# Kernel tuning notes

Hardware: AMD Instinct MI355X
Metric: run time of the kernel (lower is better)

The kernel has to match this reference:

```python
import jax, jax.numpy as jnp
import numpy as np

N = 50000  # nodes per ntype (must be equal across ntypes per the module's forward)
E = 400000  # edges per relation

# relation order matches __init__: (src_ntype, dst_ntype)
RELS = [("stock","financial"),("stock","macro"),("stock","news"),("stock","policy"),
        ("financial","macro"),("financial","stock"),("financial","news"),("financial","policy"),
        ("macro","stock"),("macro","financial"),("macro","news"),("macro","policy"),
        ("news","stock"),("news","financial"),("news","macro"),("news","policy"),
        ("policy","stock"),("policy","macro"),("policy","news"),("policy","financial")]
NTYPES = ["stock","financial","macro","news","policy"]


def graph_conv(x_src, src, dst, W, b):
    # DGL GraphConv, norm='both': h = D_in^{-1/2} A D_out^{-1/2} x W + b
    ones = jnp.ones((src.shape[0],), x_src.dtype)
    deg_out = jax.ops.segment_sum(ones, src, num_segments=N)
    norm_s = jax.lax.rsqrt(jnp.maximum(deg_out, 1.0))
    h = x_src * norm_s[:, None]
    if W.shape[0] > W.shape[1]:  # mult W first when in_feats > out_feats
        h = h @ W
        agg = jax.ops.segment_sum(h[src], dst, num_segments=N)
    else:
        agg = jax.ops.segment_sum(h[src], dst, num_segments=N)
        agg = agg @ W
    deg_in = jax.ops.segment_sum(ones, dst, num_segments=N)
    norm_d = jax.lax.rsqrt(jnp.maximum(deg_in, 1.0))
    return agg * norm_d[:, None] + b


def hetero_layer(feats, edges, W_per_rel, b_per_rel):
    # sum-aggregate per destination ntype (aggregate='sum')
    out = {nt: jnp.zeros((N, b_per_rel[0].shape[0]), jnp.float32) for nt in NTYPES}
    for r, (s_nt, d_nt) in enumerate(RELS):
        out[d_nt] = out[d_nt] + graph_conv(feats[s_nt], edges[r, 0], edges[r, 1], W_per_rel[r], b_per_rel[r])
    return out


def setup_inputs() -> dict:
    key = jax.random.key(0)
    ks = jax.random.split(key, 16)
    H, C = 128, 10
    d = {
        "x_stock": jax.random.normal(ks[0], (N, 5), jnp.float32),
        "x_financial": jax.random.normal(ks[1], (N, 16), jnp.float32),
        "x_macro": jax.random.normal(ks[2], (N, 21), jnp.float32),
        "x_news": jax.random.normal(ks[3], (N, 768), jnp.float32),
        "x_policy": jax.random.normal(ks[4], (N, 768), jnp.float32),
        "W1_stock": jax.random.normal(ks[5], (4, 5, H), jnp.float32) * 0.1,
        "W1_financial": jax.random.normal(ks[6], (4, 16, H), jnp.float32) * 0.1,
        "W1_macro": jax.random.normal(ks[7], (4, 21, H), jnp.float32) * 0.1,
        "W1_news": jax.random.normal(ks[8], (4, 768, H), jnp.float32) * 0.02,
        "W1_policy": jax.random.normal(ks[9], (4, 768, H), jnp.float32) * 0.02,
        "b1": jnp.zeros((20, H), jnp.float32),
        "W2": jax.random.normal(ks[10], (20, H, H), jnp.float32) * 0.05,
        "b2": jnp.zeros((20, H), jnp.float32),
        "Wfc": jax.random.normal(ks[11], (H, C), jnp.float32) * 0.05,
        "bfc": jnp.zeros((C,), jnp.float32),
        "edges": jax.random.randint(ks[12], (20, 2, E), 0, N, dtype=jnp.int32),
    }
    return d


def reference(x_stock, x_financial, x_macro, x_news, x_policy,
              W1_stock, W1_financial, W1_macro, W1_news, W1_policy, b1,
              W2, b2, Wfc, bfc, edges):
    feats = {"stock": x_stock, "financial": x_financial, "macro": x_macro,
             "news": x_news, "policy": x_policy}
    # layer-1 weights in relation order (RELS grouped by src ntype, 4 each)
    W1_by_src = {"stock": W1_stock, "financial": W1_financial, "macro": W1_macro,
                 "news": W1_news, "policy": W1_policy}
    W1_list = [W1_by_src[s][r % 4] for r, (s, _) in enumerate(RELS)]
    b1_list = [b1[r] for r in range(20)]
    h1 = hetero_layer(feats, edges, W1_list, b1_list)
    W2_list = [W2[r] for r in range(20)]
    b2_list = [b2[r] for r in range(20)]
    h2 = hetero_layer(h1, edges, W2_list, b2_list)
    # manual cross-ntype accumulation into stock buffer, then divide by #ntypes
    acc = h2["stock"]
    for nt in NTYPES:
        if nt != "stock":
            acc = acc + h2[nt]
    acc = acc / len(NTYPES)
    # dgl.mean_nodes over a single graph -> [1, H]
    m = jnp.mean(acc, axis=0, keepdims=True)
    out = m @ Wfc + bfc
    return (m, out)
```

## Files before the change

### kernel.cpp

```cpp
#include <hip/hip_runtime.h>

#define NN 50000
#define EE 400000

#define CH_H 32768
#define NCH_H 2
#define ESL_H 2
#define EPS_H (EE/ESL_H)
#define I4_H (EPS_H/4)

#define ESL_C 4
#define EPS_C (EE/ESL_C)
#define I4_C (EPS_C/4)

#define CH_D 8192
#define NCH_D 7
#define ESL_D 2
#define EPS_D (EE/ESL_D)
#define I4_D (EPS_D/4)

#define NZ 261
#define ZROWS 192

#define VCH 96

__constant__ int DSTT[20]     = {1,2,3,4, 2,0,3,4, 0,1,3,4, 0,1,2,4, 0,2,3,1};
__constant__ int KIDX[20]     = {0,0,0,0, 1,0,1,1, 1,1,2,2, 2,2,2,3, 3,3,3,3};
__constant__ int DSTREL[5][4] = {{5,8,12,16},{0,9,13,19},{1,4,14,17},{2,6,10,18},{3,7,11,15}};
__constant__ int FEATS[5]     = {5, 16, 21, 768, 768};

#define OFF_HIST 0
#define OFF_CRAW 0
#define OFF_CC4  0
#define OFF_C    4000000
#define OFF_ND   5000000
#define OFF_PART 0
#define OFF_YS   6500000
#define OFF_S    6600000
#define OFF_V    6700000
#define OFF_NS   7000000
#define OFF_DACC 8000000
#define DSLICE   4000000
#define OFF_Y    8000000
#define OFF_MP   8110000
#define TOTAL_ELEMS 16000000

static __device__ __forceinline__ void fma4(float4& a, const float4& x, float w) {
    a.x += w * x.x; a.y += w * x.y; a.z += w * x.z; a.w += w * x.w;
}

__global__ __launch_bounds__(1024) void k_hist(const int* __restrict__ edges, int* __restrict__ hist_part) {
    __shared__ int h[CH_H];
    const int slice = blockIdx.x, chunk = blockIdx.y;
    const int r = blockIdx.z % 20, arr = blockIdx.z / 20;
    for (int i = threadIdx.x; i < CH_H; i += 1024) h[i] = 0;
    __syncthreads();
    const int4* key = (const int4*)(edges + (size_t)(r*2 + arr)*EE + slice*EPS_H);
    const int base = chunk * CH_H;
    for (int i = threadIdx.x; i < I4_H; i += 1024) {
        int4 k4 = key[i];
        unsigned a = (unsigned)(k4.x - base), b = (unsigned)(k4.y - base);
        unsigned c = (unsigned)(k4.z - base), d = (unsigned)(k4.w - base);
        if (a < CH_H) atomicAdd(&h[a], 1);
        if (b < CH_H) atomicAdd(&h[b], 1);
        if (c < CH_H) atomicAdd(&h[c], 1);
        if (d < CH_H) atomicAdd(&h[d], 1);
    }
    __syncthreads();
    int* outp = hist_part + (arr*ESL_H + slice)*1000000 + r*NN;
    for (int i = threadIdx.x; i < CH_H; i += 1024) {
        int u = base + i;
        if (u < NN) outp[u] = h[i];
    }
}

__global__ __launch_bounds__(256) void k_norms(const int* __restrict__ hist_part,
                                               float* __restrict__ ns, float* __restrict__ nd) {
    int r = blockIdx.y;
    int u = blockIdx.x * 256 + threadIdx.x;
    if (u >= NN) return;
    int idx = r*NN + u;
    float dop = (float)(hist_part[idx] + hist_part[1000000 + idx]);
    float dip = (float)(hist_part[2000000 + idx] + hist_part[3000000 + idx]);
    if (dop < 1.f) dop = 1.f;
    if (dip < 1.f) dip = 1.f;
    ns[idx] = 1.0f / sqrtf(dop);
    nd[idx] = 1.0f / sqrtf(dip);
}

__global__ __launch_bounds__(1024) void k_craw(const int* __restrict__ edges,
                                               const float* __restrict__ nd, float* __restrict__ craw_part) {
    __shared__ float h[CH_H];
    const int slice = blockIdx.x, chunk = blockIdx.y, r = blockIdx.z;
    for (int i = threadIdx.x; i < CH_H; i += 1024) h[i] = 0.f;
    __syncthreads();
    const int4* s4 = (const int4*)(edges + (size_t)(r*2)*EE + slice*EPS_C);
    const int4* d4 = (const int4*)(edges + (size_t)(r*2+1)*EE + slice*EPS_C);
    const float* ndr = nd + r*NN;
    const int base = chunk * CH_H;
    for (int i = threadIdx.x; i < I4_C; i += 1024) {
        int4 s = s4[i];
        int4 d = d4[i];
        unsigned a = (unsigned)(s.x - base), b = (unsigned)(s.y - base);
        unsigned c = (unsigned)(s.z - base), e = (unsigned)(s.w - base);
        if (a < CH_H) atomicAdd(&h[a], ndr[d.x]);
        if (b < CH_H) atomicAdd(&h[b], ndr[d.y]);
        if (c < CH_H) atomicAdd(&h[c], ndr[d.z]);
        if (e < CH_H) atomicAdd(&h[e], ndr[d.w]);
    }
    __syncthreads();
    float* outp = craw_part + slice*1000000 + r*NN;
    for (int i = threadIdx.x; i < CH_H; i += 1024) {
        int u = base + i;
        if (u < NN) outp[u] = h[i];
    }
}

__global__ __launch_bounds__(256) void k_cS(const float* __restrict__ craw_part, const float* __restrict__ ns,
                                            float* __restrict__ c, float* __restrict__ S) {
    int r = blockIdx.y;
    int u = blockIdx.x * 256 + threadIdx.x;
    float val = 0.f;
    if (u < NN) {
        int idx = r*NN + u;
        val = ns[idx] * (craw_part[idx] + craw_part[1000000 + idx]
                       + craw_part[2000000 + idx] + craw_part[3000000 + idx]);
        c[idx] = val;
    }
    for (int off = 32; off > 0; off >>= 1) val += __shfl_down(val, off, 64);
    __shared__ float red[4];
    if ((threadIdx.x & 63) == 0) red[threadIdx.x >> 6] = val;
    __syncthreads();
    if (threadIdx.x == 0) atomicAdd(&S[r], red[0] + red[1] + red[2] + red[3]);
}

__global__ __launch_bounds__(256) void k_cc(const float* __restrict__ c, const float* __restrict__ nd,
                                            float* __restrict__ cc4) {
    int r1 = blockIdx.y;
    int u = blockIdx.x * 256 + threadIdx.x;
    if (u >= NN) return;
    float ndv = nd[r1*NN + u];
    int d1 = DSTT[r1];
    float4 w;
    w.x = c[(4*d1+0)*NN + u] * ndv;
    w.y = c[(4*d1+1)*NN + u] * ndv;
    w.z = c[(4*d1+2)*NN + u] * ndv;
    w.w = c[(4*d1+3)*NN + u] * ndv;
    *(float4*)(cc4 + (size_t)(r1*NN + u) * 4) = w;
}

__global__ __launch_bounds__(1024) void k_dacc(const int* __restrict__ edges,
                                               const float* __restrict__ cc4, float* __restrict__ dacc_part) {
    __shared__ float h4[CH_D * 4];
    const int slice = blockIdx.x, chunk = blockIdx.y, r = blockIdx.z;
    for (int i = threadIdx.x; i < CH_D * 4; i += 1024) h4[i] = 0.f;
    __syncthreads();
    const int4* s4 = (const int4*)(edges + (size_t)(r*2)*EE + slice*EPS_D);
    const int4* d4 = (const int4*)(edges + (size_t)(r*2+1)*EE + slice*EPS_D);
    const float* ccr = cc4 + (size_t)r*NN*4;
    const int base = chunk * CH_D;
    for (int i = threadIdx.x; i < I4_D; i += 1024) {
        int4 s = s4[i];
        int4 d = d4[i];
        unsigned a = (unsigned)(s.x - base), b = (unsigned)(s.y - base);
        unsigned c = (unsigned)(s.z - base), e = (unsigned)(s.w - base);
        if (a < CH_D) {
            const float4 w = *(const float4*)(ccr + (size_t)d.x * 4);
            atomicAdd(&h4[a*4+0], w.x); atomicAdd(&h4[a*4+1], w.y);
            atomicAdd(&h4[a*4+2], w.z); atomicAdd(&h4[a*4+3], w.w);
        }
        if (b < CH_D) {
            const float4 w = *(const float4*)(ccr + (size_t)d.y * 4);
            atomicAdd(&h4[b*4+0], w.x); atomicAdd(&h4[b*4+1], w.y);
            atomicAdd(&h4[b*4+2], w.z); atomicAdd(&h4[b*4+3], w.w);
        }
        if (c < CH_D) {
            const float4 w = *(const float4*)(ccr + (size_t)d.z * 4);
            atomicAdd(&h4[c*4+0], w.x); atomicAdd(&h4[c*4+1], w.y);
            atomicAdd(&h4[c*4+2], w.z); atomicAdd(&h4[c*4+3], w.w);
        }
        if (e < CH_D) {
            const float4 w = *(const float4*)(ccr + (size_t)d.w * 4);
            atomicAdd(&h4[e*4+0], w.x); atomicAdd(&h4[e*4+1], w.y);
            atomicAdd(&h4[e*4+2], w.z); atomicAdd(&h4[e*4+3], w.w);
        }
    }
    __syncthreads();
    const int d1 = DSTT[r], kk = KIDX[r];
    float* op = dacc_part + slice * DSLICE;
#pragma unroll
    for (int j = 0; j < 4; ++j) {
        int p = 4*(4*d1 + j) + kk;
        float* pj = op + (size_t)p*NN;
        for (int i = threadIdx.x; i < CH_D; i += 1024) {
            int u = base + i;
            if (u < NN) pj[u] = h4[i*4 + j];
        }
    }
}

__global__ __launch_bounds__(192) void k_y_big(const float* __restrict__ xn, const float* __restrict__ xp,
        const float* __restrict__ ns, const float* __restrict__ dacc, float* __restrict__ partial) {
    __shared__ float wlds[64 * 8];
    const int tid = threadIdx.x;
    const int z = blockIdx.x, half = blockIdx.y, group = blockIdx.z;
    const int s1 = 3 + group;
    const float* x = (group == 0) ? xn : xp;
    const int c0 = tid * 4;
    float4 acc[8];
#pragma unroll
    for (int q = 0; q < 8; ++q) acc[q] = make_float4(0.f, 0.f, 0.f, 0.f);

    for (int t = 0; t < 3; ++t) {
        const int u0 = z * ZROWS + t * 64;
        __syncthreads();
        for (int tt = tid; tt < 512; tt += 192) {
            int ql = tt >> 6, ri = tt & 63;
            int i = half*2 + (ql >> 2), j = ql & 3;
            int r1 = 4*s1 + i;
            int p = 4*(4*DSTT[r1] + j) + KIDX[r1];
            int u = u0 + ri;
            float w = 0.f;
            if (u < NN) {
                int idx = p*NN + u;
                w = ns[r1*NN + u] * (dacc[idx] + dacc[DSLICE + idx]);
            }
            wlds[ri*8 + ql] = w;
        }
        __syncthreads();
        const int rmax = (NN - u0 < 64) ? (NN - u0) : 64;
#pragma unroll 4
        for (int ri = 0; ri < rmax; ++ri) {
            const float4 xv = *(const float4*)(x + (size_t)(u0 + ri) * 768 + c0);
            const float4 wa = *(const float4*)(wlds + ri * 8);
            const float4 wb = *(const float4*)(wlds + ri * 8 + 4);
            fma4(acc[0], xv, wa.x); fma4(acc[1], xv, wa.y);
            fma4(acc[2], xv, wa.z); fma4(acc[3], xv, wa.w);
            fma4(acc[4], xv, wb.x); fma4(acc[5], xv, wb.y);
            fma4(acc[6], xv, wb.z); fma4(acc[7], xv, wb.w);
        }
    }
    float* pslot = partial + (size_t)(z*4 + group*2 + half) * 6144;
#pragma unroll
    for (int ql = 0; ql < 8; ++ql)
        *(float4*)(pslot + ql * 768 + c0) = acc[ql];
}

template<int F>
__global__ __launch_bounds__(256) void k_y_small(const float* __restrict__ x,
        const float* __restrict__ ns, const float* __restrict__ dacc,
        float* __restrict__ ys, int s1) {
    const int q = blockIdx.x;
    const int i = q >> 2, j = q & 3;
    const int r1 = 4*s1 + i;
    const int p = 4*(4*DSTT[r1] + j) + KIDX[r1];
    const float* nsp = ns + r1*NN;
    const float* d0 = dacc + (size_t)p*NN;
    const float* d1 = d0 + DSLICE;
    float acc[F];
#pragma unroll
    for (int f = 0; f < F; ++f) acc[f] = 0.f;
    const int u0 = blockIdx.y * 6250;
    for (int u = u0 + threadIdx.x; u < u0 + 6250; u += 256) {
        float w = nsp[u] * (d0[u] + d1[u]);
        const float* xr = x + (size_t)u * F;
#pragma unroll
        for (int f = 0; f < F; ++f) acc[f] += w * xr[f];
    }
#pragma unroll
    for (int f = 0; f < F; ++f)
        for (int off = 32; off > 0; off >>= 1) acc[f] += __shfl_down(acc[f], off, 64);
    __shared__ float red[F];
    if (threadIdx.x < F) red[threadIdx.x] = 0.f;
    __syncthreads();
    if ((threadIdx.x & 63) == 0) {
#pragma unroll
        for (int f = 0; f < F; ++f) atomicAdd(&red[f], acc[f]);
    }
    __syncthreads();
    if (threadIdx.x < F) atomicAdd(&ys[p*768 + threadIdx.x], red[threadIdx.x]);
}

__global__ __launch_bounds__(768) void k_red_y(const float* __restrict__ partial,
                                               const float* __restrict__ ys, float* __restrict__ y) {
    const int p = blockIdx.x;
    const int f = threadIdx.x;
    const int r2 = p >> 2, k = p & 3;
    const int r1 = DSTREL[r2 >> 2][k];
    const int s1 = r1 >> 2;
    float s = ys[p*768 + f];
    if (s1 >= 3) {
        const int group = s1 - 3;
        const int i = r1 & 3;
        const int half = i >> 1;
        const int ql = (i & 1) * 4 + (r2 & 3);
        const float* base = partial + (size_t)(group*2 + half) * 6144 + ql * 768 + f;
        for (int z = 0; z < NZ; ++z) s += base[(size_t)z * 4 * 6144];
    }
    y[p*768 + f] = s;
}

__global__ __launch_bounds__(128) void k_v(const float* __restrict__ y,
        const float* __restrict__ W1s, const float* __restrict__ W1f, const float* __restrict__ W1m,
        const float* __restrict__ W1n, const float* __restrict__ W1p, float* __restrict__ v) {
    const int r2 = blockIdx.x;
    const int k  = blockIdx.y;
    const int fc = blockIdx.z;
    const int c  = threadIdx.x;
    const int r1 = DSTREL[r2 >> 2][k];
    const int s1 = r1 >> 2;
    const int F  = FEATS[s1];
    const int f0 = fc * VCH;
    if (f0 >= F) return;
    const int f1 = (f0 + VCH < F) ? (f0 + VCH) : F;
    const float* W1 = (s1 == 0 ? W1s : s1 == 1 ? W1f : s1 == 2 ? W1m : s1 == 3 ? W1n : W1p)
                      + (size_t)(r1 & 3) * F * 128;
    const float* yp = y + (r2*4 + k) * 768;
    float sum = 0.f;
#pragma unroll 4
    for (int f = f0; f < f1; ++f) sum += yp[f] * W1[(size_t)f * 128 + c];
    atomicAdd(&v[r2 * 128 + c], sum);
}

__global__ __launch_bounds__(128) void k_m(const float* __restrict__ v, const float* __restrict__ S,
        const float* __restrict__ b1, const float* __restrict__ W2, float* __restrict__ mpart) {
    int r2 = blockIdx.x;
    int c = threadIdx.x;
    __shared__ float vp[128];
    int s2 = r2 >> 2;
    float b = b1[DSTREL[s2][0]*128 + c] + b1[DSTREL[s2][1]*128 + c]
            + b1[DSTREL[s2][2]*128 + c] + b1[DSTREL[s2][3]*128 + c];
    vp[c] = v[r2*128 + c] + S[r2] * b;
    __syncthreads();
    const float* W2r = W2 + r2 * 16384;
    float sum = 0.f;
    for (int k = 0; k < 128; ++k) sum += vp[k] * W2r[k * 128 + c];
    mpart[r2 * 128 + c] = sum;
}

__global__ __launch_bounds__(128) void k_out(const float* __restrict__ mpart, const float* __restrict__ b2,
        const float* __restrict__ Wfc, const float* __restrict__ bfc, float* __restrict__ out) {
    int c = threadIdx.x;
    __shared__ float ml[128];
    float bs = 0.f, ms = 0.f;
    for (int r2 = 0; r2 < 20; ++r2) { bs += b2[r2 * 128 + c]; ms += mpart[r2 * 128 + c]; }
    float m = (ms + (float)NN * bs) * (1.0f / (5.0f * (float)NN));
    out[c] = m;
    ml[c] = m;
    __syncthreads();
    if (c < 10) {
        float o = bfc[c];
        for (int k = 0; k < 128; ++k) o += ml[k] * Wfc[k * 10 + c];
        out[128 + c] = o;
    }
}

extern "C" void kernel_launch(void* const* d_in, const int* in_sizes, int n_in,
                              void* d_out, int out_size, void* d_ws, size_t ws_size,
                              hipStream_t stream) {
    (void)in_sizes; (void)n_in; (void)out_size;
    const float* xs  = (const float*)d_in[0];
    const float* xf  = (const float*)d_in[1];
    const float* xm  = (const float*)d_in[2];
    const float* xn  = (const float*)d_in[3];
    const float* xp  = (const float*)d_in[4];
    const float* W1s = (const float*)d_in[5];
    const float* W1f = (const float*)d_in[6];
    const float* W1m = (const float*)d_in[7];
    const float* W1n = (const float*)d_in[8];
    const float* W1p = (const float*)d_in[9];
    const float* b1  = (const float*)d_in[10];
    const float* W2  = (const float*)d_in[11];
    const float* b2  = (const float*)d_in[12];
    const float* Wfc = (const float*)d_in[13];
    const float* bfc = (const float*)d_in[14];
    const int* edges = (const int*)d_in[15];
    float* ws = (float*)d_ws;
    int* wsi = (int*)d_ws;
    float* out = (float*)d_out;
    if (ws_size < (size_t)TOTAL_ELEMS * 4) return;

    dim3 t256(256), nb(196, 20);

    hipMemsetAsync(ws + OFF_YS, 0, (size_t)(OFF_S + 64 - OFF_YS) * 4, stream);
    hipMemsetAsync(ws + OFF_V, 0, 2560 * 4, stream);

    k_hist<<<dim3(ESL_H, NCH_H, 40), dim3(1024), 0, stream>>>(edges, wsi + OFF_HIST);
    k_norms<<<nb, t256, 0, stream>>>(wsi + OFF_HIST, ws + OFF_NS, ws + OFF_ND);
    k_craw<<<dim3(ESL_C, NCH_H, 20), dim3(1024), 0, stream>>>(edges, ws + OFF_ND, ws + OFF_CRAW);
    k_cS<<<nb, t256, 0, stream>>>(ws + OFF_CRAW, ws + OFF_NS, ws + OFF_C, ws + OFF_S);
    k_cc<<<nb, t256, 0, stream>>>(ws + OFF_C, ws + OFF_ND, ws + OFF_CC4);
    k_dacc<<<dim3(ESL_D, NCH_D, 20), dim3(1024), 0, stream>>>(edges, ws + OFF_CC4, ws + OFF_DACC);
    k_y_big<<<dim3(NZ, 2, 2), dim3(192), 0, stream>>>(xn, xp, ws + OFF_NS, ws + OFF_DACC, ws + OFF_PART);
    k_y_small<5><<<dim3(16, 8), t256, 0, stream>>>(xs, ws + OFF_NS, ws + OFF_DACC, ws + OFF_YS, 0);
    k_y_small<16><<<dim3(16, 8), t256, 0, stream>>>(xf, ws + OFF_NS, ws + OFF_DACC, ws + OFF_YS, 1);
    k_y_small<21><<<dim3(16, 8), t256, 0, stream>>>(xm, ws + OFF_NS, ws + OFF_DACC, ws + OFF_YS, 2);
    k_red_y<<<dim3(80), dim3(768), 0, stream>>>(ws + OFF_PART, ws + OFF_YS, ws + OFF_Y);
    k_v<<<dim3(20, 4, 8), dim3(128), 0, stream>>>(ws + OFF_Y, W1s, W1f, W1m, W1n, W1p, ws + OFF_V);
    k_m<<<dim3(20), dim3(128), 0, stream>>>(ws + OFF_V, ws + OFF_S, b1, W2, ws + OFF_MP);
    k_out<<<dim3(1), dim3(128), 0, stream>>>(ws + OFF_MP, b2, Wfc, bfc, out);
}
```

Measured before the change: 963.3 us.

## Use direct global atomics for dacc and fuse y_big halves into one pass

The shared-memory chunked histogram in the dacc stage, which rescanned the edge lists once per chunk and wrote two partial slices, is replaced by a single pass of float atomics straight into a zeroed global buffer. The 768-wide feature reduction now handles all 16 weight columns per block instead of two halves of 8, so each large feature matrix is streamed once rather than twice. This removes repeated edge reads and the double-slice sum. In exchange it relies on global atomic throughput, adds a memset of the dacc buffer, and doubles the accumulator registers in k_y_big.

```diff
diff --git a/kernel.cpp b/kernel.cpp
--- a/kernel.cpp
+++ b/kernel.cpp
@@ -13,11 +13,8 @@
 #define EPS_C (EE/ESL_C)
 #define I4_C (EPS_C/4)
 
-#define CH_D 8192
-#define NCH_D 7
-#define ESL_D 2
-#define EPS_D (EE/ESL_D)
-#define I4_D (EPS_D/4)
+#define DBLK 80
+#define DI4  1250
 
 #define NZ 261
 #define ZROWS 192
@@ -40,7 +37,6 @@
 #define OFF_V    6700000
 #define OFF_NS   7000000
 #define OFF_DACC 8000000
-#define DSLICE   4000000
 #define OFF_Y    8000000
 #define OFF_MP   8110000
 #define TOTAL_ELEMS 16000000
@@ -149,100 +145,82 @@
     *(float4*)(cc4 + (size_t)(r1*NN + u) * 4) = w;
 }
 
-__global__ __launch_bounds__(1024) void k_dacc(const int* __restrict__ edges,
-                                               const float* __restrict__ cc4, float* __restrict__ dacc_part) {
-    __shared__ float h4[CH_D * 4];
-    const int slice = blockIdx.x, chunk = blockIdx.y, r = blockIdx.z;
-    for (int i = threadIdx.x; i < CH_D * 4; i += 1024) h4[i] = 0.f;
-    __syncthreads();
-    const int4* s4 = (const int4*)(edges + (size_t)(r*2)*EE + slice*EPS_D);
-    const int4* d4 = (const int4*)(edges + (size_t)(r*2+1)*EE + slice*EPS_D);
+__global__ __launch_bounds__(256) void k_dacc_a(const int* __restrict__ edges,
+                                                const float* __restrict__ cc4, float* __restrict__ dacc) {
+    const int blk = blockIdx.x, r = blockIdx.y;
+    const int4* s4 = (const int4*)(edges + (size_t)(r*2)*EE) + blk*DI4;
+    const int4* d4 = (const int4*)(edges + (size_t)(r*2+1)*EE) + blk*DI4;
     const float* ccr = cc4 + (size_t)r*NN*4;
-    const int base = chunk * CH_D;
-    for (int i = threadIdx.x; i < I4_D; i += 1024) {
+    const int d1 = DSTT[r], kk = KIDX[r];
+    float* b0 = dacc + (size_t)(4*(4*d1+0)+kk)*NN;
+    float* b1 = dacc + (size_t)(4*(4*d1+1)+kk)*NN;
+    float* b2 = dacc + (size_t)(4*(4*d1+2)+kk)*NN;
+    float* b3 = dacc + (size_t)(4*(4*d1+3)+kk)*NN;
+    for (int i = threadIdx.x; i < DI4; i += 256) {
         int4 s = s4[i];
         int4 d = d4[i];
-        unsigned a = (unsigned)(s.x - base), b = (unsigned)(s.y - base);
-        unsigned c = (unsigned)(s.z - base), e = (unsigned)(s.w - base);
-        if (a < CH_D) {
-            const float4 w = *(const float4*)(ccr + (size_t)d.x * 4);
-            atomicAdd(&h4[a*4+0], w.x); atomicAdd(&h4[a*4+1], w.y);
-            atomicAdd(&h4[a*4+2], w.z); atomicAdd(&h4[a*4+3], w.w);
-        }
-        if (b < CH_D) {
-            const float4 w = *(const float4*)(ccr + (size_t)d.y * 4);
-            atomicAdd(&h4[b*4+0], w.x); atomicAdd(&h4[b*4+1], w.y);
-            atomicAdd(&h4[b*4+2], w.z); atomicAdd(&h4[b*4+3], w.w);
-        }
-        if (c < CH_D) {
-            const float4 w = *(const float4*)(ccr + (size_t)d.z * 4);
-            atomicAdd(&h4[c*4+0], w.x); atomicAdd(&h4[c*4+1], w.y);
-            atomicAdd(&h4[c*4+2], w.z); atomicAdd(&h4[c*4+3], w.w);
-        }
-        if (e < CH_D) {
-            const float4 w = *(const float4*)(ccr + (size_t)d.w * 4);
-            atomicAdd(&h4[e*4+0], w.x); atomicAdd(&h4[e*4+1], w.y);
-            atomicAdd(&h4[e*4+2], w.z); atomicAdd(&h4[e*4+3], w.w);
-        }
-    }
-    __syncthreads();
-    const int d1 = DSTT[r], kk = KIDX[r];
-    float* op = dacc_part + slice * DSLICE;
-#pragma unroll
-    for (int j = 0; j < 4; ++j) {
-        int p = 4*(4*d1 + j) + kk;
-        float* pj = op + (size_t)p*NN;
-        for (int i = threadIdx.x; i < CH_D; i += 1024) {
-            int u = base + i;
-            if (u < NN) pj[u] = h4[i*4 + j];
-        }
+        {   const float4 w = *(const float4*)(ccr + (size_t)d.x * 4);
+            unsafeAtomicAdd(&b0[s.x], w.x); unsafeAtomicAdd(&b1[s.x], w.y);
+            unsafeAtomicAdd(&b2[s.x], w.z); unsafeAtomicAdd(&b3[s.x], w.w); }
+        {   const float4 w = *(const float4*)(ccr + (size_t)d.y * 4);
+            unsafeAtomicAdd(&b0[s.y], w.x); unsafeAtomicAdd(&b1[s.y], w.y);
+            unsafeAtomicAdd(&b2[s.y], w.z); unsafeAtomicAdd(&b3[s.y], w.w); }
+        {   const float4 w = *(const float4*)(ccr + (size_t)d.z * 4);
+            unsafeAtomicAdd(&b0[s.z], w.x); unsafeAtomicAdd(&b1[s.z], w.y);
+            unsafeAtomicAdd(&b2[s.z], w.z); unsafeAtomicAdd(&b3[s.z], w.w); }
+        {   const float4 w = *(const float4*)(ccr + (size_t)d.w * 4);
+            unsafeAtomicAdd(&b0[s.w], w.x); unsafeAtomicAdd(&b1[s.w], w.y);
+            unsafeAtomicAdd(&b2[s.w], w.z); unsafeAtomicAdd(&b3[s.w], w.w); }
     }
 }
 
 __global__ __launch_bounds__(192) void k_y_big(const float* __restrict__ xn, const float* __restrict__ xp,
         const float* __restrict__ ns, const float* __restrict__ dacc, float* __restrict__ partial) {
-    __shared__ float wlds[64 * 8];
+    __shared__ float wlds[64 * 16];
     const int tid = threadIdx.x;
-    const int z = blockIdx.x, half = blockIdx.y, group = blockIdx.z;
+    const int z = blockIdx.x, group = blockIdx.y;
     const int s1 = 3 + group;
     const float* x = (group == 0) ? xn : xp;
     const int c0 = tid * 4;
-    float4 acc[8];
-#pragma unroll
-    for (int q = 0; q < 8; ++q) acc[q] = make_float4(0.f, 0.f, 0.f, 0.f);
+    float4 acc[16];
+#pragma unroll
+    for (int q = 0; q < 16; ++q) acc[q] = make_float4(0.f, 0.f, 0.f, 0.f);
 
     for (int t = 0; t < 3; ++t) {
         const int u0 = z * ZROWS + t * 64;
         __syncthreads();
-        for (int tt = tid; tt < 512; tt += 192) {
+        for (int tt = tid; tt < 1024; tt += 192) {
             int ql = tt >> 6, ri = tt & 63;
-            int i = half*2 + (ql >> 2), j = ql & 3;
+            int i = ql >> 2, j = ql & 3;
             int r1 = 4*s1 + i;
             int p = 4*(4*DSTT[r1] + j) + KIDX[r1];
             int u = u0 + ri;
             float w = 0.f;
-            if (u < NN) {
-                int idx = p*NN + u;
-                w = ns[r1*NN + u] * (dacc[idx] + dacc[DSLICE + idx]);
-            }
-            wlds[ri*8 + ql] = w;
+            if (u < NN) w = ns[r1*NN + u] * dacc[p*NN + u];
+            wlds[ri*16 + ql] = w;
         }
         __syncthreads();
         const int rmax = (NN - u0 < 64) ? (NN - u0) : 64;
 #pragma unroll 4
         for (int ri = 0; ri < rmax; ++ri) {
             const float4 xv = *(const float4*)(x + (size_t)(u0 + ri) * 768 + c0);
-            const float4 wa = *(const float4*)(wlds + ri * 8);
-            const float4 wb = *(const float4*)(wlds + ri * 8 + 4);
-            fma4(acc[0], xv, wa.x); fma4(acc[1], xv, wa.y);
-            fma4(acc[2], xv, wa.z); fma4(acc[3], xv, wa.w);
-            fma4(acc[4], xv, wb.x); fma4(acc[5], xv, wb.y);
-            fma4(acc[6], xv, wb.z); fma4(acc[7], xv, wb.w);
+            const float4 wa = *(const float4*)(wlds + ri * 16);
+            const float4 wb = *(const float4*)(wlds + ri * 16 + 4);
+            const float4 wc = *(const float4*)(wlds + ri * 16 + 8);
+            const float4 wd = *(const float4*)(wlds + ri * 16 + 12);
+            fma4(acc[0],  xv, wa.x); fma4(acc[1],  xv, wa.y);
+            fma4(acc[2],  xv, wa.z); fma4(acc[3],  xv, wa.w);
+            fma4(acc[4],  xv, wb.x); fma4(acc[5],  xv, wb.y);
+            fma4(acc[6],  xv, wb.z); fma4(acc[7],  xv, wb.w);
+            fma4(acc[8],  xv, wc.x); fma4(acc[9],  xv, wc.y);
+            fma4(acc[10], xv, wc.z); fma4(acc[11], xv, wc.w);
+            fma4(acc[12], xv, wd.x); fma4(acc[13], xv, wd.y);
+            fma4(acc[14], xv, wd.z); fma4(acc[15], xv, wd.w);
         }
     }
-    float* pslot = partial + (size_t)(z*4 + group*2 + half) * 6144;
-#pragma unroll
-    for (int ql = 0; ql < 8; ++ql)
+    float* pslot = partial + (size_t)(z*2 + group) * 12288;
+#pragma unroll
+    for (int ql = 0; ql < 16; ++ql)
         *(float4*)(pslot + ql * 768 + c0) = acc[ql];
 }
 
@@ -256,13 +234,12 @@
     const int p = 4*(4*DSTT[r1] + j) + KIDX[r1];
     const float* nsp = ns + r1*NN;
     const float* d0 = dacc + (size_t)p*NN;
-    const float* d1 = d0 + DSLICE;
     float acc[F];
 #pragma unroll
     for (int f = 0; f < F; ++f) acc[f] = 0.f;
     const int u0 = blockIdx.y * 6250;
     for (int u = u0 + threadIdx.x; u < u0 + 6250; u += 256) {
-        float w = nsp[u] * (d0[u] + d1[u]);
+        float w = nsp[u] * d0[u];
         const float* xr = x + (size_t)u * F;
 #pragma unroll
         for (int f = 0; f < F; ++f) acc[f] += w * xr[f];
@@ -292,10 +269,9 @@
     if (s1 >= 3) {
         const int group = s1 - 3;
         const int i = r1 & 3;
-        const int half = i >> 1;
-        const int ql = (i & 1) * 4 + (r2 & 3);
-        const float* base = partial + (size_t)(group*2 + half) * 6144 + ql * 768 + f;
-        for (int z = 0; z < NZ; ++z) s += base[(size_t)z * 4 * 6144];
+        const int ql = i * 4 + (r2 & 3);
+        const float* base = partial + (size_t)group * 12288 + ql * 768 + f;
+        for (int z = 0; z < NZ; ++z) s += base[(size_t)z * 2 * 12288];
     }
     y[p*768 + f] = s;
 }
@@ -384,14 +360,15 @@
 
     hipMemsetAsync(ws + OFF_YS, 0, (size_t)(OFF_S + 64 - OFF_YS) * 4, stream);
     hipMemsetAsync(ws + OFF_V, 0, 2560 * 4, stream);
+    hipMemsetAsync(ws + OFF_DACC, 0, (size_t)4000000 * 4, stream);
 
     k_hist<<<dim3(ESL_H, NCH_H, 40), dim3(1024), 0, stream>>>(edges, wsi + OFF_HIST);
     k_norms<<<nb, t256, 0, stream>>>(wsi + OFF_HIST, ws + OFF_NS, ws + OFF_ND);
     k_craw<<<dim3(ESL_C, NCH_H, 20), dim3(1024), 0, stream>>>(edges, ws + OFF_ND, ws + OFF_CRAW);
     k_cS<<<nb, t256, 0, stream>>>(ws + OFF_CRAW, ws + OFF_NS, ws + OFF_C, ws + OFF_S);
     k_cc<<<nb, t256, 0, stream>>>(ws + OFF_C, ws + OFF_ND, ws + OFF_CC4);
-    k_dacc<<<dim3(ESL_D, NCH_D, 20), dim3(1024), 0, stream>>>(edges, ws + OFF_CC4, ws + OFF_DACC);
-    k_y_big<<<dim3(NZ, 2, 2), dim3(192), 0, stream>>>(xn, xp, ws + OFF_NS, ws + OFF_DACC, ws + OFF_PART);
+    k_dacc_a<<<dim3(DBLK, 20), t256, 0, stream>>>(edges, ws + OFF_CC4, ws + OFF_DACC);
+    k_y_big<<<dim3(NZ, 2), dim3(192), 0, stream>>>(xn, xp, ws + OFF_NS, ws + OFF_DACC, ws + OFF_PART);
     k_y_small<5><<<dim3(16, 8), t256, 0, stream>>>(xs, ws + OFF_NS, ws + OFF_DACC, ws + OFF_YS, 0);
     k_y_small<16><<<dim3(16, 8), t256, 0, stream>>>(xf, ws + OFF_NS, ws + OFF_DACC, ws + OFF_YS, 1);
     k_y_small<21><<<dim3(16, 8), t256, 0, stream>>>(xm, ws + OFF_NS, ws + OFF_DACC, ws + OFF_YS, 2);
```

Measured after the change: 2.275 ms. 2.36x slower.
